# Performance work log

Measured on AMD Instinct MI355X. Metric: run time of the kernel, lower is better.

The kernel has to match this reference:

```python
import jax, jax.numpy as jnp
import numpy as np

N = 50000      # num_nodes
E = 1600000    # num_edges (avg degree 32)
F_IN = 512     # in_features
F_OUT = 64     # out_features
C = 4          # num_cores


def setup_inputs() -> dict:
    key = jax.random.key(0)
    ks = jax.random.split(key, 5)
    x = jax.random.normal(ks[0], (N, F_IN), jnp.float32)
    edge_index = jax.random.randint(ks[1], (2, E), 0, N, dtype=jnp.int32)
    # KokaoCore.signal modeled as tanh(w . v + b) -> scalar, one (w, b) per core
    core_w = jax.random.normal(ks[2], (C, F_IN), jnp.float32) / np.sqrt(F_IN)
    core_b = jnp.zeros((C,), jnp.float32)
    # output_transform: nn.Linear(num_cores, out_features)
    W_out = jax.random.normal(ks[3], (F_OUT, C), jnp.float32) / np.sqrt(C)
    b_out = jnp.zeros((F_OUT,), jnp.float32)
    return {"x": x, "edge_index": edge_index, "core_w": core_w,
            "core_b": core_b, "W_out": W_out, "b_out": b_out}


def reference(x, edge_index, core_w, core_b, W_out, b_out):
    src, tgt = edge_index[0], edge_index[1]
    # per-node, per-core scalar signal (computed once per node, gathered per edge)
    s = jnp.tanh(x @ core_w.T + core_b)                              # (N, C)
    seg_sum = jax.ops.segment_sum(s[src], tgt, num_segments=N)       # (N, C)
    count = jax.ops.segment_sum(jnp.ones((E,), x.dtype), tgt, num_segments=N)  # (N,)
    # mean over neighbors; nodes with no in-edges stay zero (torch.zeros init)
    avg = jnp.where(count[:, None] > 0, seg_sum / jnp.maximum(count, 1.0)[:, None], 0.0)
    # aggregated[i] = avg_signal * x[i][:out_features], stacked over cores on last dim
    messages = avg[:, None, :] * x[:, :F_OUT, None]                  # (N, F_OUT, C)
    out = jnp.einsum('nfc,oc->nfo', messages, W_out) + b_out         # (N, F_OUT, F_OUT)
    return jax.nn.relu(out)
```

## Files before the change

kernel.cpp:

```cpp
#include <hip/hip_runtime.h>

#define F_IN 512
#define F_OUT 64
#define NB_SHIFT 7
#define NB_MAX 512
#define CAP_B 5120
#define P_CHUNK 8192

typedef float v4f __attribute__((ext_vector_type(4)));
typedef unsigned int uint32;
typedef unsigned long long u64;


__global__ __launch_bounds__(256) void signal_kernel(
    const float* __restrict__ x, const float* __restrict__ core_w,
    const float* __restrict__ core_b, float* __restrict__ s,
    uint32* __restrict__ gcur, int N, int nb) {
  if (blockIdx.x == 0) {
    for (int b = threadIdx.x; b < nb; b += 256) gcur[b] = 0;
  }

  int wave = (int)((blockIdx.x * blockDim.x + threadIdx.x) >> 6);
  int lane = threadIdx.x & 63;
  if (wave >= N) return;

  const v4f* xv = (const v4f*)(x + (size_t)wave * F_IN);
  v4f a0 = xv[lane * 2];
  v4f a1 = xv[lane * 2 + 1];

  float p[4];
#pragma unroll
  for (int c = 0; c < 4; ++c) {
    const v4f* wv = (const v4f*)(core_w + c * F_IN);
    v4f w0 = wv[lane * 2];
    v4f w1 = wv[lane * 2 + 1];
    p[c] = a0.x * w0.x + a0.y * w0.y + a0.z * w0.z + a0.w * w0.w +
           a1.x * w1.x + a1.y * w1.y + a1.z * w1.z + a1.w * w1.w;
  }
#pragma unroll
  for (int off = 32; off > 0; off >>= 1) {
#pragma unroll
    for (int c = 0; c < 4; ++c) p[c] += __shfl_down(p[c], off, 64);
  }
  if (lane == 0) {
    v4f r;
    r.x = tanhf(p[0] + core_b[0]);
    r.y = tanhf(p[1] + core_b[1]);
    r.z = tanhf(p[2] + core_b[2]);
    r.w = tanhf(p[3] + core_b[3]);
    ((v4f*)s)[wave] = r;
  }
}

__global__ __launch_bounds__(256) void part_kernel(
    const int* __restrict__ src, const int* __restrict__ tgt,
    uint32* __restrict__ gcur, uint32* __restrict__ grec, int E, int nb) {
  __shared__ uint32 hist[NB_MAX];
  __shared__ uint32 cur[NB_MAX];
  int tid = threadIdx.x;
  int start = (int)blockIdx.x * P_CHUNK;
  int end = start + P_CHUNK;
  if (end > E) end = E;

  for (int b = tid; b < nb; b += 256) hist[b] = 0;
  __syncthreads();

  for (int i = start + tid; i < end; i += 256)
    atomicAdd(&hist[(uint32)tgt[i] >> NB_SHIFT], 1u);
  __syncthreads();

  for (int b = tid; b < nb; b += 256) {
    uint32 t = hist[b];
    cur[b] = t ? atomicAdd(&gcur[b], t) : 0u;
  }
  __syncthreads();

  for (int i = start + tid; i < end; i += 256) {
    uint32 v = (uint32)tgt[i];
    uint32 u = (uint32)src[i];
    uint32 b = v >> NB_SHIFT;
    uint32 pos = atomicAdd(&cur[b], 1u);
    if (pos < CAP_B) grec[(size_t)b * CAP_B + pos] = (v & 127u) | (u << 7);
  }
}

__global__ __launch_bounds__(256) void agg_kernel(
    const float* __restrict__ s, const uint32* __restrict__ gcur,
    const uint32* __restrict__ grec, float* __restrict__ avg, int N) {
  int b = blockIdx.x;
  int tid = threadIdx.x;
  __shared__ u64 accA[128];
  __shared__ u64 accB[128];

  if (tid < 128) { accA[tid] = 0ull; accB[tid] = 0ull; }
  __syncthreads();

  uint32 cnt = gcur[b];
  if (cnt > CAP_B) cnt = CAP_B;
  const uint32* rp = grec + (size_t)b * CAP_B;
  for (uint32 r = tid; r < cnt; r += 256) {
    uint32 rec = rp[r];
    uint32 node = rec & 127u;
    uint32 u = rec >> 7;
    v4f sv = ((const v4f*)s)[u];
    uint32 q0 = (uint32)__float2int_rn((sv.x + 1.0f) * 8388608.0f);
    uint32 q1 = (uint32)__float2int_rn((sv.y + 1.0f) * 8388608.0f);
    uint32 q2 = (uint32)__float2int_rn((sv.z + 1.0f) * 8388608.0f);
    uint32 q3 = (uint32)__float2int_rn((sv.w + 1.0f) * 131072.0f);
    atomicAdd(&accA[node], (u64)q0 | ((u64)q1 << 32));
    atomicAdd(&accB[node], (u64)q2 | ((u64)(q3 | (1u << 25)) << 32));
  }
  __syncthreads();

  int n = (b << NB_SHIFT) | tid;
  if (tid < 128 && n < N) {
    u64 wa = accA[tid];
    u64 wb = accB[tid];
    uint32 deg = (uint32)(wb >> 57);
    uint32 f3  = (uint32)(wb >> 32) & 0x1ffffffu;
    float fdeg = (float)deg;
    float inv = deg ? 1.0f / fdeg : 0.0f;
    v4f a;
    a.x = ((float)(uint32)wa         * 0x1p-23f - fdeg) * inv;
    a.y = ((float)(uint32)(wa >> 32) * 0x1p-23f - fdeg) * inv;
    a.z = ((float)(uint32)wb         * 0x1p-23f - fdeg) * inv;
    a.w = ((float)f3                 * 0x1p-17f - fdeg) * inv;
    ((v4f*)avg)[n] = a;
  }
}

__global__ __launch_bounds__(256) void out_kernel(
    const float* __restrict__ x, const float* __restrict__ avg,
    const float* __restrict__ W_out, const float* __restrict__ b_out,
    float* __restrict__ out, int N) {
  int lane = threadIdx.x & 63;
  int gwave = (int)((blockIdx.x * blockDim.x + threadIdx.x) >> 6);
  int nwaves = (int)((gridDim.x * blockDim.x) >> 6);
  int col = lane & 15;

  v4f w0 = ((const v4f*)W_out)[col * 4 + 0];
  v4f w1 = ((const v4f*)W_out)[col * 4 + 1];
  v4f w2 = ((const v4f*)W_out)[col * 4 + 2];
  v4f w3 = ((const v4f*)W_out)[col * 4 + 3];
  v4f bq = ((const v4f*)b_out)[col];

  for (int n = gwave; n < N; n += nwaves) {
    v4f a = ((const v4f*)avg)[n];

    float t0 = a.x * w0.x + a.y * w0.y + a.z * w0.z + a.w * w0.w;
    float t1 = a.x * w1.x + a.y * w1.y + a.z * w1.z + a.w * w1.w;
    float t2 = a.x * w2.x + a.y * w2.y + a.z * w2.z + a.w * w2.w;
    float t3 = a.x * w3.x + a.y * w3.y + a.z * w3.z + a.w * w3.w;

    float xval = x[(size_t)n * F_IN + lane];

    v4f* ov = (v4f*)(out + (size_t)n * (F_OUT * F_OUT));
#pragma unroll
    for (int it = 0; it < 16; ++it) {
      float xf = __shfl(xval, (lane >> 4) + it * 4, 64);
      v4f r;
      r.x = fmaxf(xf * t0 + bq.x, 0.0f);
      r.y = fmaxf(xf * t1 + bq.y, 0.0f);
      r.z = fmaxf(xf * t2 + bq.z, 0.0f);
      r.w = fmaxf(xf * t3 + bq.w, 0.0f);
      ov[lane + it * 64] = r;
    }
  }
}

extern "C" void kernel_launch(void* const* d_in, const int* in_sizes, int n_in,
                              void* d_out, int out_size, void* d_ws, size_t ws_size,
                              hipStream_t stream) {
  const float* x      = (const float*)d_in[0];
  const int*   eidx   = (const int*)d_in[1];
  const float* core_w = (const float*)d_in[2];
  const float* core_b = (const float*)d_in[3];
  const float* W_out  = (const float*)d_in[4];
  const float* b_out  = (const float*)d_in[5];
  float* out = (float*)d_out;

  const int N = in_sizes[0] / F_IN;
  const int E = in_sizes[1] / 2;
  const int* src = eidx;
  const int* tgt = eidx + E;
  const int nb = (N + 127) >> NB_SHIFT;

  float*  s    = (float*)d_ws;
  float*  avg  = s + (size_t)N * 4;
  uint32* gcur = (uint32*)(avg + (size_t)N * 4);
  uint32* grec = gcur + NB_MAX;

  signal_kernel<<<(N + 3) / 4, 256, 0, stream>>>(x, core_w, core_b, s, gcur, N, nb);
  {
    int blocks = (E + P_CHUNK - 1) / P_CHUNK;
    part_kernel<<<blocks, 256, 0, stream>>>(src, tgt, gcur, grec, E, nb);
  }
  agg_kernel<<<nb, 256, 0, stream>>>(s, gcur, grec, avg, N);
  out_kernel<<<2048, 256, 0, stream>>>(x, avg, W_out, b_out, out, N);
}
```

Measured before the change: 940.5 us.

## Locally sort edge records in shared memory before coalesced global scatter

```diff
diff --git a/kernel.cpp b/kernel.cpp
--- a/kernel.cpp
+++ b/kernel.cpp
@@ -56,22 +56,40 @@
     const int* __restrict__ src, const int* __restrict__ tgt,
     uint32* __restrict__ gcur, uint32* __restrict__ grec, int E, int nb) {
   __shared__ uint32 hist[NB_MAX];
-  __shared__ uint32 cur[NB_MAX];
+  __shared__ uint32 scan[NB_MAX];
+  __shared__ uint32 delta[NB_MAX];
+  __shared__ uint32 sorted[P_CHUNK];
+  __shared__ unsigned short sbkt[P_CHUNK];
   int tid = threadIdx.x;
   int start = (int)blockIdx.x * P_CHUNK;
   int end = start + P_CHUNK;
   if (end > E) end = E;
 
-  for (int b = tid; b < nb; b += 256) hist[b] = 0;
+  for (int b = tid; b < NB_MAX; b += 256) hist[b] = 0;
   __syncthreads();
 
   for (int i = start + tid; i < end; i += 256)
     atomicAdd(&hist[(uint32)tgt[i] >> NB_SHIFT], 1u);
   __syncthreads();
 
+  scan[tid] = hist[tid];
+  scan[tid + 256] = hist[tid + 256];
+  __syncthreads();
+  for (int off = 1; off < NB_MAX; off <<= 1) {
+    uint32 v0 = (tid >= off) ? scan[tid - off] : 0u;
+    uint32 v1 = scan[tid + 256 - off];
+    __syncthreads();
+    scan[tid] += v0;
+    scan[tid + 256] += v1;
+    __syncthreads();
+  }
+
   for (int b = tid; b < nb; b += 256) {
-    uint32 t = hist[b];
-    cur[b] = t ? atomicAdd(&gcur[b], t) : 0u;
+    uint32 cntb = hist[b];
+    uint32 ls = b ? scan[b - 1] : 0u;
+    uint32 gb = cntb ? atomicAdd(&gcur[b], cntb) : 0u;
+    delta[b] = (uint32)b * CAP_B + gb - ls;
+    hist[b] = ls;
   }
   __syncthreads();
 
@@ -79,8 +97,17 @@
     uint32 v = (uint32)tgt[i];
     uint32 u = (uint32)src[i];
     uint32 b = v >> NB_SHIFT;
-    uint32 pos = atomicAdd(&cur[b], 1u);
-    if (pos < CAP_B) grec[(size_t)b * CAP_B + pos] = (v & 127u) | (u << 7);
+    uint32 lpos = atomicAdd(&hist[b], 1u);
+    sorted[lpos] = (v & 127u) | (u << 7);
+    sbkt[lpos] = (unsigned short)b;
+  }
+  __syncthreads();
+
+  int cnt = end - start;
+  for (int i = tid; i < cnt; i += 256) {
+    uint32 b = sbkt[i];
+    uint32 gdst = delta[b] + (uint32)i;
+    if (gdst < (b + 1u) * CAP_B) grec[gdst] = sorted[i];
   }
 }
 
```

New measurement: 932.0 us. About the same (-0.9%).
